# Kernel tuning notes

Hardware: AMD Instinct MI355X
Metric: run time of the kernel (lower is better)

Reference implementation:

```python
import jax, jax.numpy as jnp
import numpy as np

EPS = 1e-5
NUM_GROUPS = 16


def _deform_conv(x, offset, mask, weight):
    """Modulated deformable conv v2, 3x3, stride 1, pad 1, no bias.
    x: [B,C,H,W], offset: [B,18,H,W] (y,x interleaved per kernel point),
    mask: [B,9,H,W], weight: [O,C,3,3].
    """
    B, C, H, W = x.shape
    O = weight.shape[0]
    K = 9
    off = offset.reshape(B, K, 2, H, W)
    dy, dx = off[:, :, 0], off[:, :, 1]  # [B,K,H,W]
    # base sampling grid: output pixel + kernel tap offset (pad=1 -> taps -1..1)
    ky, kx = jnp.meshgrid(jnp.arange(3), jnp.arange(3), indexing='ij')
    ky = (ky.reshape(K) - 1).astype(x.dtype)
    kx = (kx.reshape(K) - 1).astype(x.dtype)
    iy = jnp.arange(H, dtype=x.dtype)[:, None]
    ix = jnp.arange(W, dtype=x.dtype)[None, :]
    py = iy[None, None] + ky[None, :, None, None] + dy  # [B,K,H,W]
    px = ix[None, None] + kx[None, :, None, None] + dx

    y0 = jnp.floor(py)
    x0 = jnp.floor(px)
    wy = py - y0  # grad flows to offsets via these weights
    wx = px - x0

    xf = x.reshape(B, C, H * W)

    def gather(yc, xc, w):
        # yc,xc,w: [B,K,H,W] float; returns weighted samples [B,C,K,H,W]
        valid = (yc >= 0) & (yc <= H - 1) & (xc >= 0) & (xc <= W - 1)
        yi = jnp.clip(yc, 0, H - 1).astype(jnp.int32)
        xi = jnp.clip(xc, 0, W - 1).astype(jnp.int32)
        idx = (yi * W + xi).reshape(B, K * H * W)
        g = jax.vmap(lambda xb, ib: xb[:, ib])(xf, idx)  # [B,C,K*H*W]
        g = g.reshape(B, C, K, H, W)
        wv = (w * valid.astype(x.dtype))[:, None]  # [B,1,K,H,W]
        return g * wv

    val = gather(y0, x0, (1 - wy) * (1 - wx))
    val = val + gather(y0, x0 + 1, (1 - wy) * wx)
    val = val + gather(y0 + 1, x0, wy * (1 - wx))
    val = val + gather(y0 + 1, x0 + 1, wy * wx)

    val = val * mask[:, None]  # modulation: [B,C,K,H,W] * [B,1,K,H,W]
    w = weight.reshape(O, C, K)
    return jnp.einsum('bckhw,ock->bohw', val, w)


def _group_norm(y, gamma, beta):
    B, O, H, W = y.shape
    g = y.reshape(B, NUM_GROUPS, O // NUM_GROUPS, H, W)
    mean = g.mean(axis=(2, 3, 4), keepdims=True)
    var = ((g - mean) ** 2).mean(axis=(2, 3, 4), keepdims=True)
    g = (g - mean) * jax.lax.rsqrt(var + EPS)
    y = g.reshape(B, O, H, W)
    return y * gamma[None, :, None, None] + beta[None, :, None, None]


def setup_inputs() -> dict:
    key = jax.random.key(0)
    k1, k2, k3, k4 = jax.random.split(key, 4)
    B, C, O, H, W = 8, 256, 256, 64, 64
    x = jax.random.normal(k1, (B, C, H, W), jnp.float32)
    offset = jax.random.normal(k2, (B, 18, H, W), jnp.float32)
    mask = jax.random.uniform(k3, (B, 9, H, W), jnp.float32)
    weight = jax.random.normal(k4, (O, C, 3, 3), jnp.float32) * 0.02
    gamma = jnp.ones((O,), jnp.float32)
    beta = jnp.zeros((O,), jnp.float32)
    return {"x": x, "offset": offset, "mask": mask, "weight": weight,
            "gamma": gamma, "beta": beta}


def reference(x, offset, mask, weight, gamma, beta):
    y = _deform_conv(x, offset, mask, weight)
    return _group_norm(y, gamma, beta)
```

## Files before the change

kernel.cpp:

```cpp
#include <hip/hip_runtime.h>
#include <hip/hip_fp16.h>
#include <math.h>

#define BB 8
#define CC 256
#define OO 256
#define HH 64
#define WW 64
#define KK 9
#define HWSZ 4096
#define CKSZ 2304
#define NG 16
#define OPG 16
#define EPSV 1e-5f

typedef _Float16 f16;
typedef f16 f16x8 __attribute__((ext_vector_type(8)));
typedef float f32x4 __attribute__((ext_vector_type(4)));

#define XH_ELEMS ((size_t)BB*HWSZ*CC)
#define WH_ELEMS ((size_t)OO*CKSZ)
#define POUT_ELEMS ((size_t)BB*OO*HWSZ)
#define WS_NEED_SPLIT ((XH_ELEMS + WH_ELEMS + 2*POUT_ELEMS)*2 + 1024)

__device__ __forceinline__ void gload_lds16(const void* g, void* l) {
  __builtin_amdgcn_global_load_lds(
      (const __attribute__((address_space(1))) void*)g,
      (__attribute__((address_space(3))) void*)l, 16, 0, 0);
}

__global__ __launch_bounds__(256) void x_transpose_k(
    const float* __restrict__ x, __half* __restrict__ xh)
{
  int blk = blockIdx.x;
  int b = blk >> 8; int rem = blk & 255;
  int c0 = (rem >> 6) * 64; int hw0 = (rem & 63) * 64;
  __shared__ float st[64][65];
  int t = threadIdx.x;
  #pragma unroll
  for (int i = 0; i < 16; ++i) {
    int idx = t + i*256; int c = idx >> 6, w = idx & 63;
    st[c][w] = x[((size_t)(b*CC + c0 + c))*HWSZ + hw0 + w];
  }
  __syncthreads();
  #pragma unroll
  for (int i = 0; i < 8; ++i) {
    int idx = t + i*256; int r = idx >> 5, cp = idx & 31;
    __half2 v = __floats2half2_rn(st[cp*2][r], st[cp*2+1][r]);
    *(__half2*)&xh[((size_t)(b*HWSZ) + hw0 + r)*CC + c0 + cp*2] = v;
  }
}

__global__ __launch_bounds__(256) void w_reorder_k(
    const float* __restrict__ w, __half* __restrict__ wh)
{
  int i = blockIdx.x*256 + threadIdx.x;
  int o = i / CKSZ; int kp = i - o*CKSZ;
  int kk = kp >> 8, c = kp & 255;
  wh[i] = __float2half(w[o*CKSZ + c*KK + kk]);
}

template<int SPLIT>
__global__ __launch_bounds__(512, 4) void dcn_mfma_k(
    const float* __restrict__ off, const float* __restrict__ msk,
    const __half* __restrict__ xh, const __half* __restrict__ wh,
    float* __restrict__ out, __half* __restrict__ pout)
{
  __shared__ __half sWl[OO*64];
  __shared__ __half sVl[128*64];
  __shared__ uint    sTapOff[128][4];
  __shared__ __half2 sTapW [128][4];

  const int t = threadIdx.x;
  const int b = blockIdx.x & 7;
  const int rest = blockIdx.x >> 3;
  const int kh    = SPLIT ? (rest & 1) : 0;
  const int strip = SPLIT ? (rest >> 1) : rest;
  const int h0 = strip * 2;
  const int cstart = SPLIT ? kh*18 : 0;
  const int nch    = SPLIT ? 18 : 36;

  const int lane = t & 63, wid = t >> 6;
  const int wm = wid & 3, wn = wid >> 2;
  const int lr = lane & 15, lh = lane >> 4;

  f32x4 acc[4][4];
  #pragma unroll
  for (int mi = 0; mi < 4; ++mi)
    #pragma unroll
    for (int ni = 0; ni < 4; ++ni) acc[mi][ni] = (f32x4){0.f, 0.f, 0.f, 0.f};

  const char* xbase = (const char*)xh + (size_t)b * (HWSZ*CC*2);
  int kprev = -1;

  for (int cc = cstart; cc < cstart + nch; ++cc) {
    const int k = cc >> 2;
    const int c0 = (cc & 3) << 6;
    __syncthreads();

    if (k != kprev) {
      kprev = k;
      if (t < 128) {
        int p = t;
        int h = h0 + (p >> 6), w = p & 63;
        float dy = off[(((b*18) + 2*k    )*HH + h)*WW + w];
        float dx = off[(((b*18) + 2*k + 1)*HH + h)*WW + w];
        float m  = msk[(((b*KK) + k)*HH + h)*WW + w];
        float py = (float)(h + (k/3) - 1) + dy;
        float px = (float)(w + (k%3) - 1) + dx;
        float y0f = floorf(py), x0f = floorf(px);
        float wy = py - y0f, wx = px - x0f;
        int y0 = (int)y0f, x0 = (int)x0f;
        #pragma unroll
        for (int tap = 0; tap < 4; ++tap) {
          int yy = y0 + (tap >> 1), xx = x0 + (tap & 1);
          bool v = (yy >= 0) & (yy < HH) & (xx >= 0) & (xx < WW);
          float bw = ((tap >> 1) ? wy : 1.f - wy) * ((tap & 1) ? wx : 1.f - wx);
          float wgt = v ? bw * m : 0.f;
          int cy = min(max(yy, 0), HH-1), cx = min(max(xx, 0), WW-1);
          sTapOff[p][tap] = (uint)((cy*WW + cx) * (CC*2));
          sTapW [p][tap] = __float2half2_rn(wgt);
        }
      }
      __syncthreads();
    }

    {
      #pragma unroll
      for (int i = 0; i < 4; ++i) {
        int idx = i*512 + t;
        int o = idx >> 3, s = idx & 7;
        const __half* g = wh + (size_t)o*CKSZ + k*256 + c0 + ((s ^ (o & 7)) << 3);
        char* ldsbase = (char*)sWl + (size_t)(i*512 + (t & ~63))*16;
        gload_lds16(g, ldsbase);
      }
    }
    {
      int p = t >> 2, q = t & 3;
      const uint4 offs = *(const uint4*)&sTapOff[p][0];
      __half2 w0 = sTapW[p][0], w1 = sTapW[p][1],
              w2 = sTapW[p][2], w3 = sTapW[p][3];
      const char* cb = xbase + (size_t)(c0*2);
      #pragma unroll
      for (int i = 0; i < 2; ++i) {
        int oct = q + i*4;
        int boff = oct * 16;
        uint4 r0 = *(const uint4*)(cb + offs.x + boff);
        uint4 r1 = *(const uint4*)(cb + offs.y + boff);
        uint4 r2 = *(const uint4*)(cb + offs.z + boff);
        uint4 r3 = *(const uint4*)(cb + offs.w + boff);
        const __half2* t0 = (const __half2*)&r0;
        const __half2* t1 = (const __half2*)&r1;
        const __half2* t2 = (const __half2*)&r2;
        const __half2* t3 = (const __half2*)&r3;
        __half2 o_[4];
        #pragma unroll
        for (int r = 0; r < 4; ++r)
          o_[r] = __hfma2(w0, t0[r],
                  __hfma2(w1, t1[r],
                  __hfma2(w2, t2[r], __hmul2(w3, t3[r]))));
        int s = oct ^ (p & 7);
        *(uint4*)&sVl[p*64 + s*8] = *(uint4*)o_;
      }
    }
    __syncthreads();
    #pragma unroll
    for (int ks = 0; ks < 2; ++ks) {
      f16x8 a[4], bfr[4];
      #pragma unroll
      for (int mi = 0; mi < 4; ++mi) {
        int r = wm*64 + mi*16 + lr;
        a[mi] = *(const f16x8*)&sWl[r*64 + (((ks*4 + lh) ^ (r & 7)) << 3)];
      }
      #pragma unroll
      for (int ni = 0; ni < 4; ++ni) {
        int r = wn*64 + ni*16 + lr;
        bfr[ni] = *(const f16x8*)&sVl[r*64 + (((ks*4 + lh) ^ (r & 7)) << 3)];
      }
      #pragma unroll
      for (int mi = 0; mi < 4; ++mi)
        #pragma unroll
        for (int ni = 0; ni < 4; ++ni)
          acc[mi][ni] = __builtin_amdgcn_mfma_f32_16x16x32_f16(
              a[mi], bfr[ni], acc[mi][ni], 0, 0, 0);
    }
  }

  #pragma unroll
  for (int mi = 0; mi < 4; ++mi) {
    #pragma unroll
    for (int ni = 0; ni < 4; ++ni) {
      int ob = wm*64 + mi*16 + lh*4;
      int pp = wn*64 + ni*16 + lr;
      if (SPLIT) {
        __half* dst = pout + (size_t)kh*POUT_ELEMS;
        #pragma unroll
        for (int j = 0; j < 4; ++j)
          dst[((size_t)(b*OO + ob + j))*HWSZ + h0*WW + pp] =
              __float2half(acc[mi][ni][j]);
      } else {
        #pragma unroll
        for (int j = 0; j < 4; ++j)
          out[((size_t)(b*OO + ob + j))*HWSZ + h0*WW + pp] = acc[mi][ni][j];
      }
    }
  }
}

__global__ __launch_bounds__(1024) void reduce_stats_k(
    const __half* __restrict__ p0, const __half* __restrict__ p1,
    float* __restrict__ out, float* __restrict__ stats)
{
  int bg = blockIdx.x;
  size_t base = (size_t)bg * (OPG*HWSZ);
  float s1 = 0.f, s2 = 0.f;
  for (int i = threadIdx.x; i < OPG*HWSZ/8; i += 1024) {
    size_t o8 = base + (size_t)i*8;
    uint4 ua = *(const uint4*)(p0 + o8);
    uint4 ub = *(const uint4*)(p1 + o8);
    const __half2* ah = (const __half2*)&ua;
    const __half2* bh = (const __half2*)&ub;
    float r[8];
    #pragma unroll
    for (int j = 0; j < 4; ++j) {
      float2 fa = __half22float2(ah[j]);
      float2 fb = __half22float2(bh[j]);
      r[2*j]   = fa.x + fb.x;
      r[2*j+1] = fa.y + fb.y;
    }
    #pragma unroll
    for (int j = 0; j < 8; ++j) { s1 += r[j]; s2 += r[j]*r[j]; }
    *(float4*)(out + o8)     = make_float4(r[0], r[1], r[2], r[3]);
    *(float4*)(out + o8 + 4) = make_float4(r[4], r[5], r[6], r[7]);
  }
  #pragma unroll
  for (int o2 = 32; o2 > 0; o2 >>= 1) {
    s1 += __shfl_down(s1, o2);
    s2 += __shfl_down(s2, o2);
  }
  __shared__ float r1[16], r2[16];
  int wd = threadIdx.x >> 6, lane = threadIdx.x & 63;
  if (lane == 0) { r1[wd] = s1; r2[wd] = s2; }
  __syncthreads();
  if (threadIdx.x == 0) {
    float t1 = 0.f, t2 = 0.f;
    #pragma unroll
    for (int i = 0; i < 16; i++) { t1 += r1[i]; t2 += r2[i]; }
    const float invN = 1.f / (float)(OPG*HWSZ);
    float mean = t1 * invN;
    float var  = t2 * invN - mean*mean;
    stats[bg*2]   = mean;
    stats[bg*2+1] = var;
  }
}

__global__ __launch_bounds__(1024) void gn_stats_k(
    const float* __restrict__ out, float* __restrict__ stats)
{
  int bg = blockIdx.x;
  const float4* p = (const float4*)(out + (size_t)bg*OPG*HWSZ);
  const int n4 = OPG*HWSZ/4;
  float s1 = 0.f, s2 = 0.f;
  for (int i = threadIdx.x; i < n4; i += 1024) {
    float4 v = p[i];
    s1 += v.x + v.y + v.z + v.w;
    s2 += v.x*v.x + v.y*v.y + v.z*v.z + v.w*v.w;
  }
  #pragma unroll
  for (int o2 = 32; o2 > 0; o2 >>= 1) {
    s1 += __shfl_down(s1, o2);
    s2 += __shfl_down(s2, o2);
  }
  __shared__ float r1[16], r2[16];
  int wd = threadIdx.x >> 6, lane = threadIdx.x & 63;
  if (lane == 0) { r1[wd] = s1; r2[wd] = s2; }
  __syncthreads();
  if (threadIdx.x == 0) {
    float t1 = 0.f, t2 = 0.f;
    #pragma unroll
    for (int i = 0; i < 16; i++) { t1 += r1[i]; t2 += r2[i]; }
    const float invN = 1.f / (float)(OPG*HWSZ);
    float mean = t1 * invN;
    float var  = t2 * invN - mean*mean;
    stats[bg*2]   = mean;
    stats[bg*2+1] = var;
  }
}

__global__ __launch_bounds__(256) void gn_norm_k(
    float* __restrict__ out, const float* __restrict__ stats,
    const float* __restrict__ gamma, const float* __restrict__ beta)
{
  size_t i = (size_t)blockIdx.x*256 + threadIdx.x;
  const size_t n4 = (size_t)BB*OO*HWSZ/4;
  if (i >= n4) return;
  size_t base = i*4;
  int bo = (int)(base / HWSZ);
  int b = bo / OO, o = bo - b*OO;
  int g = o >> 4;
  float mean = stats[(b*NG+g)*2], var = stats[(b*NG+g)*2+1];
  float inv = rsqrtf(var + EPSV);
  float sc = gamma[o]*inv;
  float sh = beta[o] - mean*sc;
  float4 v = *(float4*)&out[base];
  v.x = v.x*sc + sh; v.y = v.y*sc + sh;
  v.z = v.z*sc + sh; v.w = v.w*sc + sh;
  *(float4*)&out[base] = v;
}

extern "C" void kernel_launch(void* const* d_in, const int* in_sizes, int n_in,
                              void* d_out, int out_size, void* d_ws, size_t ws_size,
                              hipStream_t stream) {
  const float* x      = (const float*)d_in[0];
  const float* offset = (const float*)d_in[1];
  const float* mask   = (const float*)d_in[2];
  const float* weight = (const float*)d_in[3];
  const float* gamma  = (const float*)d_in[4];
  const float* beta   = (const float*)d_in[5];
  float* out = (float*)d_out;

  __half* xh   = (__half*)d_ws;
  __half* wh   = xh + XH_ELEMS;
  __half* pout = wh + WH_ELEMS;
  float* stats = (float*)(pout + 2*POUT_ELEMS);
  float* stats_fb = (float*)(wh + WH_ELEMS);

  x_transpose_k<<<BB*4*64, 256, 0, stream>>>(x, xh);
  w_reorder_k<<<(int)(WH_ELEMS/256), 256, 0, stream>>>(weight, wh);

  if (ws_size >= WS_NEED_SPLIT) {
    dcn_mfma_k<1><<<512, 512, 0, stream>>>(offset, mask, xh, wh, out, pout);
    reduce_stats_k<<<BB*NG, 1024, 0, stream>>>(pout, pout + POUT_ELEMS, out, stats);
    gn_norm_k<<<(int)((size_t)BB*OO*HWSZ/4 + 255)/256, 256, 0, stream>>>(
        out, stats, gamma, beta);
  } else {
    dcn_mfma_k<0><<<256, 512, 0, stream>>>(offset, mask, xh, wh, out, (__half*)nullptr);
    gn_stats_k<<<BB*NG, 1024, 0, stream>>>(out, stats_fb);
    gn_norm_k<<<(int)((size_t)BB*OO*HWSZ/4 + 255)/256, 256, 0, stream>>>(
        out, stats_fb, gamma, beta);
  }
}
```

Baseline: 97.42 us.

## Split deformable conv reduction three ways and fuse partial-sum into GroupNorm normalize

Generalizes the channel-tap split of the MFMA deformable conv from 2 to 3 partial outputs (768 blocks instead of 512) and raises the occupancy hint in launch_bounds. GroupNorm statistics are now computed by many smaller blocks writing partial sums. A new normalize kernel re-reads and sums the fp16 partials directly, so the intermediate fp32 output write and re-read are dropped. The cost is an extra fp16 partial buffer plus re-reading the partials twice, and the added occupancy hint may cause register pressure or spills.

```diff
diff --git a/kernel.cpp b/kernel.cpp
--- a/kernel.cpp
+++ b/kernel.cpp
@@ -21,7 +21,6 @@
 #define XH_ELEMS ((size_t)BB*HWSZ*CC)
 #define WH_ELEMS ((size_t)OO*CKSZ)
 #define POUT_ELEMS ((size_t)BB*OO*HWSZ)
-#define WS_NEED_SPLIT ((XH_ELEMS + WH_ELEMS + 2*POUT_ELEMS)*2 + 1024)
 
 __device__ __forceinline__ void gload_lds16(const void* g, void* l) {
   __builtin_amdgcn_global_load_lds(
@@ -60,8 +59,8 @@
   wh[i] = __float2half(w[o*CKSZ + c*KK + kk]);
 }
 
-template<int SPLIT>
-__global__ __launch_bounds__(512, 4) void dcn_mfma_k(
+template<int S>
+__global__ __launch_bounds__(512, 6) void dcn_mfma_k(
     const float* __restrict__ off, const float* __restrict__ msk,
     const __half* __restrict__ xh, const __half* __restrict__ wh,
     float* __restrict__ out, __half* __restrict__ pout)
@@ -74,11 +73,11 @@
   const int t = threadIdx.x;
   const int b = blockIdx.x & 7;
   const int rest = blockIdx.x >> 3;
-  const int kh    = SPLIT ? (rest & 1) : 0;
-  const int strip = SPLIT ? (rest >> 1) : rest;
+  const int kh    = (S > 1) ? (rest % S) : 0;
+  const int strip = (S > 1) ? (rest / S) : rest;
   const int h0 = strip * 2;
-  const int cstart = SPLIT ? kh*18 : 0;
-  const int nch    = SPLIT ? 18 : 36;
+  const int cstart = kh * (36/S);
+  const int nch    = 36/S;
 
   const int lane = t & 63, wid = t >> 6;
   const int wm = wid & 3, wn = wid >> 2;
@@ -192,7 +191,7 @@
     for (int ni = 0; ni < 4; ++ni) {
       int ob = wm*64 + mi*16 + lh*4;
       int pp = wn*64 + ni*16 + lr;
-      if (SPLIT) {
+      if (S > 1) {
         __half* dst = pout + (size_t)kh*POUT_ELEMS;
         #pragma unroll
         for (int j = 0; j < 4; ++j)
@@ -207,51 +206,91 @@
   }
 }
 
-__global__ __launch_bounds__(1024) void reduce_stats_k(
-    const __half* __restrict__ p0, const __half* __restrict__ p1,
-    float* __restrict__ out, float* __restrict__ stats)
-{
-  int bg = blockIdx.x;
-  size_t base = (size_t)bg * (OPG*HWSZ);
+template<int S>
+__global__ __launch_bounds__(256) void gn_stats_part_k(
+    const __half* __restrict__ pout, float* __restrict__ psum)
+{
+  int bid = blockIdx.x;
+  int bg = bid >> 3, sub = bid & 7;
+  size_t base = (size_t)bg*(OPG*HWSZ) + (size_t)sub*8192;
   float s1 = 0.f, s2 = 0.f;
-  for (int i = threadIdx.x; i < OPG*HWSZ/8; i += 1024) {
+  for (int i = threadIdx.x; i < 1024; i += 256) {
     size_t o8 = base + (size_t)i*8;
-    uint4 ua = *(const uint4*)(p0 + o8);
-    uint4 ub = *(const uint4*)(p1 + o8);
-    const __half2* ah = (const __half2*)&ua;
-    const __half2* bh = (const __half2*)&ub;
     float r[8];
     #pragma unroll
-    for (int j = 0; j < 4; ++j) {
-      float2 fa = __half22float2(ah[j]);
-      float2 fb = __half22float2(bh[j]);
-      r[2*j]   = fa.x + fb.x;
-      r[2*j+1] = fa.y + fb.y;
+    for (int j = 0; j < 8; ++j) r[j] = 0.f;
+    #pragma unroll
+    for (int s = 0; s < S; ++s) {
+      uint4 u = *(const uint4*)(pout + (size_t)s*POUT_ELEMS + o8);
+      const __half2* h = (const __half2*)&u;
+      #pragma unroll
+      for (int j = 0; j < 4; ++j) {
+        float2 f = __half22float2(h[j]);
+        r[2*j]   += f.x;
+        r[2*j+1] += f.y;
+      }
     }
     #pragma unroll
     for (int j = 0; j < 8; ++j) { s1 += r[j]; s2 += r[j]*r[j]; }
-    *(float4*)(out + o8)     = make_float4(r[0], r[1], r[2], r[3]);
-    *(float4*)(out + o8 + 4) = make_float4(r[4], r[5], r[6], r[7]);
   }
   #pragma unroll
   for (int o2 = 32; o2 > 0; o2 >>= 1) {
     s1 += __shfl_down(s1, o2);
     s2 += __shfl_down(s2, o2);
   }
-  __shared__ float r1[16], r2[16];
+  __shared__ float r1[4], r2[4];
   int wd = threadIdx.x >> 6, lane = threadIdx.x & 63;
   if (lane == 0) { r1[wd] = s1; r2[wd] = s2; }
   __syncthreads();
   if (threadIdx.x == 0) {
-    float t1 = 0.f, t2 = 0.f;
-    #pragma unroll
-    for (int i = 0; i < 16; i++) { t1 += r1[i]; t2 += r2[i]; }
-    const float invN = 1.f / (float)(OPG*HWSZ);
-    float mean = t1 * invN;
-    float var  = t2 * invN - mean*mean;
-    stats[bg*2]   = mean;
-    stats[bg*2+1] = var;
-  }
+    float t1 = r1[0]+r1[1]+r1[2]+r1[3];
+    float t2 = r2[0]+r2[1]+r2[2]+r2[3];
+    psum[bid*2]   = t1;
+    psum[bid*2+1] = t2;
+  }
+}
+
+template<int S>
+__global__ __launch_bounds__(256) void gn_norm_part_k(
+    const __half* __restrict__ pout, const float* __restrict__ psum,
+    const float* __restrict__ gamma, const float* __restrict__ beta,
+    float* __restrict__ out)
+{
+  int bid = blockIdx.x;
+  size_t base = (size_t)bid * 2048;
+  int bo = bid >> 1;
+  int b = bo >> 8, o = bo & 255;
+  int bg = b*NG + (o >> 4);
+  float s1 = 0.f, s2 = 0.f;
+  #pragma unroll
+  for (int i = 0; i < 8; ++i) {
+    s1 += psum[(bg*8 + i)*2];
+    s2 += psum[(bg*8 + i)*2 + 1];
+  }
+  const float invN = 1.f / (float)(OPG*HWSZ);
+  float mean = s1 * invN;
+  float var  = s2 * invN - mean*mean;
+  float inv = rsqrtf(var + EPSV);
+  float sc = gamma[o]*inv;
+  float sh = beta[o] - mean*sc;
+
+  size_t e0 = base + (size_t)threadIdx.x*8;
+  float r[8];
+  #pragma unroll
+  for (int j = 0; j < 8; ++j) r[j] = 0.f;
+  #pragma unroll
+  for (int s = 0; s < S; ++s) {
+    uint4 u = *(const uint4*)(pout + (size_t)s*POUT_ELEMS + e0);
+    const __half2* h = (const __half2*)&u;
+    #pragma unroll
+    for (int j = 0; j < 4; ++j) {
+      float2 f = __half22float2(h[j]);
+      r[2*j]   += f.x;
+      r[2*j+1] += f.y;
+    }
+  }
+  *(float4*)&out[e0]     = make_float4(r[0]*sc+sh, r[1]*sc+sh, r[2]*sc+sh, r[3]*sc+sh);
+  *(float4*)&out[e0 + 4] = make_float4(r[4]*sc+sh, r[5]*sc+sh, r[6]*sc+sh, r[7]*sc+sh);
 }
 
 __global__ __launch_bounds__(1024) void gn_stats_k(
@@ -322,21 +361,28 @@
   __half* xh   = (__half*)d_ws;
   __half* wh   = xh + XH_ELEMS;
   __half* pout = wh + WH_ELEMS;
-  float* stats = (float*)(pout + 2*POUT_ELEMS);
-  float* stats_fb = (float*)(wh + WH_ELEMS);
+
+  const size_t need3 = (XH_ELEMS + WH_ELEMS + 3*POUT_ELEMS)*2 + 16384;
+  const size_t need2 = (XH_ELEMS + WH_ELEMS + 2*POUT_ELEMS)*2 + 16384;
 
   x_transpose_k<<<BB*4*64, 256, 0, stream>>>(x, xh);
   w_reorder_k<<<(int)(WH_ELEMS/256), 256, 0, stream>>>(weight, wh);
 
-  if (ws_size >= WS_NEED_SPLIT) {
-    dcn_mfma_k<1><<<512, 512, 0, stream>>>(offset, mask, xh, wh, out, pout);
-    reduce_stats_k<<<BB*NG, 1024, 0, stream>>>(pout, pout + POUT_ELEMS, out, stats);
+  if (ws_size >= need3) {
+    float* psum = (float*)(pout + 3*POUT_ELEMS);
+    dcn_mfma_k<3><<<8*3*32, 512, 0, stream>>>(offset, mask, xh, wh, out, pout);
+    gn_stats_part_k<3><<<128*8, 256, 0, stream>>>(pout, psum);
+    gn_norm_part_k<3><<<4096, 256, 0, stream>>>(pout, psum, gamma, beta, out);
+  } else if (ws_size >= need2) {
+    float* psum = (float*)(pout + 2*POUT_ELEMS);
+    dcn_mfma_k<2><<<8*2*32, 512, 0, stream>>>(offset, mask, xh, wh, out, pout);
+    gn_stats_part_k<2><<<128*8, 256, 0, stream>>>(pout, psum);
+    gn_norm_part_k<2><<<4096, 256, 0, stream>>>(pout, psum, gamma, beta, out);
+  } else {
+    float* stats = (float*)(wh + WH_ELEMS);
+    dcn_mfma_k<1><<<8*32, 512, 0, stream>>>(offset, mask, xh, wh, out, (__half*)nullptr);
+    gn_stats_k<<<BB*NG, 1024, 0, stream>>>(out, stats);
     gn_norm_k<<<(int)((size_t)BB*OO*HWSZ/4 + 255)/256, 256, 0, stream>>>(
         out, stats, gamma, beta);
-  } else {
-    dcn_mfma_k<0><<<256, 512, 0, stream>>>(offset, mask, xh, wh, out, (__half*)nullptr);
-    gn_stats_k<<<BB*NG, 1024, 0, stream>>>(out, stats_fb);
-    gn_norm_k<<<(int)((size_t)BB*OO*HWSZ/4 + 255)/256, 256, 0, stream>>>(
-        out, stats_fb, gamma, beta);
-  }
-}
+  }
+}
```

New measurement: 359.3 us. 3.69x slower.
